# Kernel tuning notes

Measured on AMD Instinct MI355X. Metric: run time of the kernel, lower is better.

The kernel has to match this reference:

```python
import jax, jax.numpy as jnp
import numpy as np

STEPS, BATCH = 2048, 512
INPUT_DIM = 16          # climate features after stripping flow channel
STORE_DIM = 8           # number of conceptual stores S
HIDDEN = 128
SLOW = 2                # SLOW_STORE index
RAIN_IDX = 0            # rain column within sliced climate inputs
OUT_DIM = STORE_DIM * (STORE_DIM + 2)   # flow_between_stores=True -> 80
IN_DIM_FLOWNET = INPUT_DIM + STORE_DIM  # 24


def setup_inputs() -> dict:
    key = jax.random.key(0)
    ks = jax.random.split(key, 10)
    hyd_input = jax.random.uniform(ks[0], (STEPS, BATCH, 1 + INPUT_DIM), dtype=jnp.float32)
    s = 0.05
    W0 = jax.random.normal(ks[1], (HIDDEN, IN_DIM_FLOWNET), dtype=jnp.float32) * s
    b0 = jax.random.normal(ks[2], (HIDDEN,), dtype=jnp.float32) * s
    W1 = jax.random.normal(ks[3], (HIDDEN, HIDDEN), dtype=jnp.float32) * s
    b1 = jax.random.normal(ks[4], (HIDDEN,), dtype=jnp.float32) * s
    W_in = jax.random.normal(ks[5], (STORE_DIM + 1, HIDDEN), dtype=jnp.float32) * s
    b_in = jax.random.normal(ks[6], (STORE_DIM + 1,), dtype=jnp.float32) * s
    W_out = jax.random.normal(ks[7], (OUT_DIM, HIDDEN), dtype=jnp.float32) * s
    b_out = jax.random.normal(ks[8], (OUT_DIM,), dtype=jnp.float32) * s - 3.0  # bias.data -= 3
    return {"hyd_input": hyd_input, "W0": W0, "b0": b0, "W1": W1, "b1": b1,
            "W_in": W_in, "b_in": b_in, "W_out": W_out, "b_out": b_out}


def reference(hyd_input, W0, b0, W1, b1, W_in, b_in, W_out, b_out):
    S = STORE_DIM
    flow = hyd_input[:, :, 0]          # [T, B] observed flow
    x = hyd_input[:, :, 1:]            # [T, B, F] climate forcings
    rain = x[:, :, RAIN_IDX]           # [T, B]
    # correct_init_baseflow: 25th percentile of observed flow over time, per batch elem
    baseflow = jnp.percentile(flow, 25.0, axis=0)  # [B]

    B = x.shape[1]
    stores0 = jnp.zeros((B, S), dtype=hyd_input.dtype).at[:, 1].set(1.0)  # init_stores

    def step(stores, inp):
        x_t, rain_t, is_first = inp
        # flownet: (num_layers=2) Linear -> ReLU (dropout is eval-mode identity)
        h = jnp.concatenate([x_t, 0.01 * stores], axis=1)      # [B, F+S]
        h = jax.nn.relu(h @ W0.T + b0)
        h = jax.nn.relu(h @ W1.T + b1)
        # inflow gating (softmax over S+1): distribute rain into stores
        a = jax.nn.softmax(h @ W_in.T + b_in, axis=-1)          # [B, S+1]
        stores = stores + a[:, 1:] * rain_t[:, None]
        # outflow fluxes (sigmoid), S*(S+2) = inter-store | escape | flow
        b = jax.nn.sigmoid(h @ W_out.T + b_out)                 # [B, S*(S+2)]
        # sequential inter-store transfers (order matters; S is small/fixed)
        for d in range(S):
            fb = b[:, d * S:(d + 1) * S] * stores               # [B, S]
            stores = (stores - fb).at[:, d].add(fb.sum(axis=1))
        escape = b[:, -2 * S:-S] * stores
        stores = stores - escape
        b_flow = b[:, -S:]
        flow_distn = b_flow * stores
        stores = stores - flow_distn
        # at i==0: overwrite slow store from baseflow / outflow coeff
        corrected = stores.at[:, SLOW].set(baseflow / jnp.maximum(b_flow[:, SLOW], 1e-5))
        stores = jnp.where(is_first, corrected, stores)
        return stores, flow_distn.sum(axis=1)

    is_first = jnp.arange(x.shape[0]) == 0
    _, flows = jax.lax.scan(step, stores0, (x, rain, is_first))
    return flows  # [T, B]
```

## Files before the change

kernel.cpp:

```cpp
#include <hip/hip_runtime.h>
#include <hip/hip_bf16.h>
#include <math.h>

#define STEPS 2048
#define BATCH 512

typedef __attribute__((ext_vector_type(8))) short short8;
typedef __attribute__((ext_vector_type(4))) short short4v;
typedef __attribute__((ext_vector_type(2))) short short2v;
typedef __attribute__((ext_vector_type(4))) float f32x4;

__device__ __forceinline__ short f2bf(float f) {
    union { float f; unsigned u; } v; v.f = f;
    unsigned u = v.u;
    return (short)((u + 0x7FFFu + ((u >> 16) & 1u)) >> 16);
}
__device__ __forceinline__ short2v pk2(float a, float b) {
    __hip_bfloat162 h = __float22bfloat162_rn(make_float2(a, b));
    union { __hip_bfloat162 h; short2v s; } u; u.h = h; return u.s;
}

__global__ __launch_bounds__(256) void baseflow_kernel(
    const float* __restrict__ hyd, float* __restrict__ bf)
{
    __shared__ float arr[STEPS];
    const int b = blockIdx.x;
    const int tid = threadIdx.x;
    for (int t = tid; t < STEPS; t += 256)
        arr[t] = hyd[(size_t)(t * BATCH + b) * 17];
    __syncthreads();
    for (int k = 2; k <= STEPS; k <<= 1) {
        for (int j = k >> 1; j > 0; j >>= 1) {
            for (int i = tid; i < STEPS; i += 256) {
                int ixj = i ^ j;
                if (ixj > i) {
                    float a = arr[i], c = arr[ixj];
                    bool up = ((i & k) == 0);
                    if (up ? (a > c) : (a < c)) { arr[i] = c; arr[ixj] = a; }
                }
            }
            __syncthreads();
        }
    }
    if (tid == 0) bf[b] = arr[511] + 0.75f * (arr[512] - arr[511]);
}

__global__ __launch_bounds__(256, 1) void hyd_step_kernel(
    const float* __restrict__ hyd,
    const float* __restrict__ W0,  const float* __restrict__ b0,
    const float* __restrict__ W1,  const float* __restrict__ b1,
    const float* __restrict__ Win, const float* __restrict__ bin,
    const float* __restrict__ Wout,const float* __restrict__ bout,
    const float* __restrict__ baseflow,
    float* __restrict__ out)
{
    __shared__ __align__(16) short h1F[256 * 8];
    __shared__ __align__(16) short h2F[256 * 8];
    __shared__ __align__(16) short ringX[16 * 4 * 8];
    __shared__ float ringR[16][2];
    __shared__ __align__(16) float hb[2][96];

    const int tid  = threadIdx.x;
    const int blk  = blockIdx.x;
    const int lane = tid & 63;
    const int wv   = tid >> 6;
    const int cn   = lane & 15;
    const int cg   = lane >> 4;
    const int col  = lane & 1;

    for (int i = tid; i < 256 * 8; i += 256) { h1F[i] = 0; h2F[i] = 0; }

    short8 a0[2]; f32x4 c0[2];
    short8 a1[2][4]; f32x4 c1[2];
    short8 ah[2][4]; f32x4 ch[2];
    #pragma unroll
    for (int i = 0; i < 2; ++i) {
        const int mt = 2 * wv + i;
        const int row = mt * 16 + cn;
        #pragma unroll
        for (int j = 0; j < 8; ++j) {
            int k = cg * 8 + j;
            a0[i][j] = (k < 24) ? f2bf(W0[row * 24 + k]) : (short)0;
        }
        #pragma unroll
        for (int kt = 0; kt < 4; ++kt)
            #pragma unroll
            for (int j = 0; j < 8; ++j)
                a1[i][kt][j] = f2bf(W1[row * 128 + kt * 32 + cg * 8 + j]);
        #pragma unroll
        for (int r = 0; r < 4; ++r) {
            int m = mt * 16 + cg * 4 + r;
            c0[i][r] = b0[m];
            c1[i][r] = b1[m];
        }
    }
    const int nht = (wv < 2) ? 2 : 1;
    int htile[2];
    htile[0] = (wv < 2) ? 2 * wv : 4 + (wv - 2);
    htile[1] = (wv < 2) ? 2 * wv + 1 : htile[0];
    #pragma unroll
    for (int i = 0; i < 2; ++i) {
        const int ht = htile[i];
        const int row = ht * 16 + cn;
        #pragma unroll
        for (int kt = 0; kt < 4; ++kt)
            #pragma unroll
            for (int j = 0; j < 8; ++j) {
                int k = kt * 32 + cg * 8 + j;
                float w = 0.f;
                if (row < 9)       w = Win[row * 128 + k];
                else if (row < 89) w = Wout[(row - 9) * 128 + k];
                ah[i][kt][j] = f2bf(w);
            }
        #pragma unroll
        for (int r = 0; r < 4; ++r) {
            int m = ht * 16 + cg * 4 + r;
            float bb = 0.f;
            if (m < 9)       bb = bin[m];
            else if (m < 89) bb = bout[m - 9];
            ch[i][r] = bb;
        }
    }

    float sreg[8];
    #pragma unroll
    for (int j = 0; j < 8; ++j) sreg[j] = (j == 1) ? 1.f : 0.f;
    const float bfv = baseflow[blk * 2 + col];
    short8 spack;
    #pragma unroll
    for (int jj = 0; jj < 4; ++jj) {
        short2v p = pk2(0.01f * sreg[2 * jj], 0.01f * sreg[2 * jj + 1]);
        spack[2 * jj] = p[0]; spack[2 * jj + 1] = p[1];
    }

    for (int tb = 0; tb < STEPS; tb += 16) {
        if (tid < 64) {
            const int tp = tid >> 2, c = (tid >> 1) & 1, g2 = tid & 1;
            const float* p = hyd + ((size_t)(tb + tp) * BATCH + blk * 2 + c) * 17 + 1 + g2 * 8;
            float v0 = p[0], v1 = p[1], v2 = p[2], v3 = p[3];
            float v4 = p[4], v5 = p[5], v6 = p[6], v7 = p[7];
            short8 w;
            short2v q0 = pk2(v0, v1), q1 = pk2(v2, v3), q2 = pk2(v4, v5), q3 = pk2(v6, v7);
            w[0] = q0[0]; w[1] = q0[1]; w[2] = q1[0]; w[3] = q1[1];
            w[4] = q2[0]; w[5] = q2[1]; w[6] = q3[0]; w[7] = q3[1];
            *(short8*)&ringX[(tp * 4 + g2 * 2 + c) * 8] = w;
        } else if (tid < 96) {
            const int l = tid - 64, tp = l >> 1, c = l & 1;
            ringR[tp][c] = hyd[((size_t)(tb + tp) * BATCH + blk * 2 + c) * 17 + 1];
        }
        __syncthreads();

        for (int tt = 0; tt < 16; ++tt) {
            const int t = tb + tt;

            const float rain = ringR[tt][col];

            short8 bfrag = 0;
            if (cn < 2) {
                if (cg < 2)        bfrag = *(const short8*)&ringX[(tt * 4 + cg * 2 + cn) * 8];
                else if (cg == 2)  bfrag = spack;
            }
            #pragma unroll
            for (int i = 0; i < 2; ++i) {
                f32x4 acc = __builtin_amdgcn_mfma_f32_16x16x32_bf16(a0[i], bfrag, c0[i], 0, 0, 0);
                if (cn < 2) {
                    int m0 = (2 * wv + i) * 16 + cg * 4;
                    short4v p;
                    short2v pa = pk2(fmaxf(acc[0], 0.f), fmaxf(acc[1], 0.f));
                    short2v pb = pk2(fmaxf(acc[2], 0.f), fmaxf(acc[3], 0.f));
                    p[0] = pa[0]; p[1] = pa[1]; p[2] = pb[0]; p[3] = pb[1];
                    *(short4v*)&h1F[((m0 >> 3) * 16 + cn) * 8 + (m0 & 7)] = p;
                }
            }
            __syncthreads();

            short8 bf1[4];
            #pragma unroll
            for (int kt = 0; kt < 4; ++kt)
                bf1[kt] = *(const short8*)&h1F[(kt * 64 + lane) * 8];
            #pragma unroll
            for (int i = 0; i < 2; ++i) {
                f32x4 acc = c1[i];
                #pragma unroll
                for (int kt = 0; kt < 4; ++kt)
                    acc = __builtin_amdgcn_mfma_f32_16x16x32_bf16(a1[i][kt], bf1[kt], acc, 0, 0, 0);
                if (cn < 2) {
                    int m0 = (2 * wv + i) * 16 + cg * 4;
                    short4v p;
                    short2v pa = pk2(fmaxf(acc[0], 0.f), fmaxf(acc[1], 0.f));
                    short2v pb = pk2(fmaxf(acc[2], 0.f), fmaxf(acc[3], 0.f));
                    p[0] = pa[0]; p[1] = pa[1]; p[2] = pb[0]; p[3] = pb[1];
                    *(short4v*)&h2F[((m0 >> 3) * 16 + cn) * 8 + (m0 & 7)] = p;
                }
            }
            __syncthreads();

            short8 bf2[4];
            #pragma unroll
            for (int kt = 0; kt < 4; ++kt)
                bf2[kt] = *(const short8*)&h2F[(kt * 64 + lane) * 8];
            #pragma unroll
            for (int i = 0; i < 2; ++i) {
                if (i < nht) {
                    f32x4 acc = ch[i];
                    #pragma unroll
                    for (int kt = 0; kt < 4; ++kt)
                        acc = __builtin_amdgcn_mfma_f32_16x16x32_bf16(ah[i][kt], bf2[kt], acc, 0, 0, 0);
                    if (cn < 2) {
                        const int ht = htile[i];
                        float4 o;
                        #pragma unroll
                        for (int r = 0; r < 4; ++r) {
                            int m = ht * 16 + cg * 4 + r;
                            float v = acc[r];
                            bool isl = (m < 9);
                            float em = __expf(isl ? v : -v);
                            float res = isl ? em : __builtin_amdgcn_rcpf(1.f + em);
                            ((float*)&o)[r] = res;
                        }
                        *(float4*)&hb[cn][ht * 16 + cg * 4] = o;
                    }
                }
            }
            __syncthreads();

            {
                float gv[92];
                const float4* hp = (const float4*)&hb[col][0];
                #pragma unroll
                for (int c2 = 0; c2 < 23; ++c2)
                    ((float4*)gv)[c2] = hp[c2];

                float den = ((gv[0] + gv[1]) + (gv[2] + gv[3])) +
                            ((gv[4] + gv[5]) + (gv[6] + gv[7])) + gv[8];
                float rr = rain * __builtin_amdgcn_rcpf(den);
                #pragma unroll
                for (int j = 0; j < 8; ++j) sreg[j] += gv[1 + j] * rr;

                #pragma unroll
                for (int d = 0; d < 8; ++d) {
                    float fb[8];
                    #pragma unroll
                    for (int j = 0; j < 8; ++j) fb[j] = gv[9 + d * 8 + j] * sreg[j];
                    float fs = ((fb[0] + fb[1]) + (fb[2] + fb[3])) +
                               ((fb[4] + fb[5]) + (fb[6] + fb[7]));
                    #pragma unroll
                    for (int j = 0; j < 8; ++j) sreg[j] -= fb[j];
                    sreg[d] += fs;
                }
                #pragma unroll
                for (int j = 0; j < 8; ++j) sreg[j] -= gv[73 + j] * sreg[j];
                float fd[8];
                #pragma unroll
                for (int j = 0; j < 8; ++j) fd[j] = gv[81 + j] * sreg[j];
                float fsum = ((fd[0] + fd[1]) + (fd[2] + fd[3])) +
                             ((fd[4] + fd[5]) + (fd[6] + fd[7]));
                #pragma unroll
                for (int j = 0; j < 8; ++j) sreg[j] -= fd[j];
                if (t == 0) sreg[2] = bfv / fmaxf(gv[83], 1e-5f);

                #pragma unroll
                for (int jj = 0; jj < 4; ++jj) {
                    short2v p = pk2(0.01f * sreg[2 * jj], 0.01f * sreg[2 * jj + 1]);
                    spack[2 * jj] = p[0]; spack[2 * jj + 1] = p[1];
                }
                if (tid < 2) out[(size_t)t * BATCH + blk * 2 + tid] = fsum;
            }
        }
    }
}

extern "C" void kernel_launch(void* const* d_in, const int* in_sizes, int n_in,
                              void* d_out, int out_size, void* d_ws, size_t ws_size,
                              hipStream_t stream)
{
    const float* hyd  = (const float*)d_in[0];
    const float* W0   = (const float*)d_in[1];
    const float* b0   = (const float*)d_in[2];
    const float* W1   = (const float*)d_in[3];
    const float* b1   = (const float*)d_in[4];
    const float* Win  = (const float*)d_in[5];
    const float* bin  = (const float*)d_in[6];
    const float* Wout = (const float*)d_in[7];
    const float* bout = (const float*)d_in[8];
    float* out = (float*)d_out;
    float* bf  = (float*)d_ws;

    baseflow_kernel<<<BATCH, 256, 0, stream>>>(hyd, bf);
    hyd_step_kernel<<<BATCH / 2, 256, 0, stream>>>(
        hyd, W0, b0, W1, b1, Win, bin, Wout, bout, bf, out);
}
```

Baseline: 3.395 ms.

## Prefetch per-step inputs into registers and precompute input-layer MFMA off critical path

Drops the shared-memory ring buffer of 16 timesteps and its extra barrier. Each lane now prefetches the next step's climate inputs and rain straight into registers. The x-part of the first-layer MFMA for step t+1 is issued during step t's scalar store update, so only the store-dependent MFMA stays on the serial recurrence. The head weights are shifted by one row so the gate outputs line up for 2-wide float vector arithmetic (packed FMA) in the sequential store update. The cost is per-step global loads with latency that must be hidden, and more live registers.

```diff
diff --git a/kernel.cpp b/kernel.cpp
--- a/kernel.cpp
+++ b/kernel.cpp
@@ -9,6 +9,7 @@
 typedef __attribute__((ext_vector_type(4))) short short4v;
 typedef __attribute__((ext_vector_type(2))) short short2v;
 typedef __attribute__((ext_vector_type(4))) float f32x4;
+typedef __attribute__((ext_vector_type(2))) float f32x2;
 
 __device__ __forceinline__ short f2bf(float f) {
     union { float f; unsigned u; } v; v.f = f;
@@ -56,9 +57,7 @@
 {
     __shared__ __align__(16) short h1F[256 * 8];
     __shared__ __align__(16) short h2F[256 * 8];
-    __shared__ __align__(16) short ringX[16 * 4 * 8];
-    __shared__ float ringR[16][2];
-    __shared__ __align__(16) float hb[2][96];
+    __shared__ __align__(16) float hb[2][100];
 
     const int tid  = threadIdx.x;
     const int blk  = blockIdx.x;
@@ -108,164 +107,208 @@
             for (int j = 0; j < 8; ++j) {
                 int k = kt * 32 + cg * 8 + j;
                 float w = 0.f;
-                if (row < 9)       w = Win[row * 128 + k];
-                else if (row < 89) w = Wout[(row - 9) * 128 + k];
+                if (row != 1) {
+                    int q = (row == 0) ? 0 : (row - 1);
+                    if (q < 9)       w = Win[q * 128 + k];
+                    else if (q < 89) w = Wout[(q - 9) * 128 + k];
+                }
                 ah[i][kt][j] = f2bf(w);
             }
         #pragma unroll
         for (int r = 0; r < 4; ++r) {
             int m = ht * 16 + cg * 4 + r;
             float bb = 0.f;
-            if (m < 9)       bb = bin[m];
-            else if (m < 89) bb = bout[m - 9];
+            if (m != 1) {
+                int q = (m == 0) ? 0 : (m - 1);
+                if (q < 9)       bb = bin[q];
+                else if (q < 89) bb = bout[q - 9];
+            }
             ch[i][r] = bb;
         }
     }
 
-    float sreg[8];
-    #pragma unroll
-    for (int j = 0; j < 8; ++j) sreg[j] = (j == 1) ? 1.f : 0.f;
+    f32x2 s01 = {0.f, 1.f}, s23 = {0.f, 0.f}, s45 = {0.f, 0.f}, s67 = {0.f, 0.f};
     const float bfv = baseflow[blk * 2 + col];
     short8 spack;
-    #pragma unroll
-    for (int jj = 0; jj < 4; ++jj) {
-        short2v p = pk2(0.01f * sreg[2 * jj], 0.01f * sreg[2 * jj + 1]);
-        spack[2 * jj] = p[0]; spack[2 * jj + 1] = p[1];
-    }
-
-    for (int tb = 0; tb < STEPS; tb += 16) {
-        if (tid < 64) {
-            const int tp = tid >> 2, c = (tid >> 1) & 1, g2 = tid & 1;
-            const float* p = hyd + ((size_t)(tb + tp) * BATCH + blk * 2 + c) * 17 + 1 + g2 * 8;
-            float v0 = p[0], v1 = p[1], v2 = p[2], v3 = p[3];
-            float v4 = p[4], v5 = p[5], v6 = p[6], v7 = p[7];
-            short8 w;
-            short2v q0 = pk2(v0, v1), q1 = pk2(v2, v3), q2 = pk2(v4, v5), q3 = pk2(v6, v7);
-            w[0] = q0[0]; w[1] = q0[1]; w[2] = q1[0]; w[3] = q1[1];
-            w[4] = q2[0]; w[5] = q2[1]; w[6] = q3[0]; w[7] = q3[1];
-            *(short8*)&ringX[(tp * 4 + g2 * 2 + c) * 8] = w;
-        } else if (tid < 96) {
-            const int l = tid - 64, tp = l >> 1, c = l & 1;
-            ringR[tp][c] = hyd[((size_t)(tb + tp) * BATCH + blk * 2 + c) * 17 + 1];
+    {
+        short2v p0 = pk2(0.01f * s01.x, 0.01f * s01.y);
+        short2v p1 = pk2(0.01f * s23.x, 0.01f * s23.y);
+        short2v p2 = pk2(0.01f * s45.x, 0.01f * s45.y);
+        short2v p3 = pk2(0.01f * s67.x, 0.01f * s67.y);
+        spack[0] = p0[0]; spack[1] = p0[1]; spack[2] = p1[0]; spack[3] = p1[1];
+        spack[4] = p2[0]; spack[5] = p2[1]; spack[6] = p3[0]; spack[7] = p3[1];
+    }
+
+    const bool xlane = (cn < 2) && (cg < 2);
+    const int xoff = (blk * 2 + cn) * 17 + 1 + cg * 8;
+    const int roff = (blk * 2 + col) * 17 + 1;
+    float xv[8];
+    float rain_next;
+    if (xlane) {
+        const float* p = hyd + xoff;
+        #pragma unroll
+        for (int j = 0; j < 8; ++j) xv[j] = p[j];
+    }
+    rain_next = hyd[roff];
+
+    f32x4 accx0, accx1;
+    {
+        short8 xfrag = 0;
+        if (xlane) {
+            short2v q0 = pk2(xv[0], xv[1]), q1 = pk2(xv[2], xv[3]),
+                    q2 = pk2(xv[4], xv[5]), q3 = pk2(xv[6], xv[7]);
+            xfrag[0] = q0[0]; xfrag[1] = q0[1]; xfrag[2] = q1[0]; xfrag[3] = q1[1];
+            xfrag[4] = q2[0]; xfrag[5] = q2[1]; xfrag[6] = q3[0]; xfrag[7] = q3[1];
+        }
+        accx0 = __builtin_amdgcn_mfma_f32_16x16x32_bf16(a0[0], xfrag, c0[0], 0, 0, 0);
+        accx1 = __builtin_amdgcn_mfma_f32_16x16x32_bf16(a0[1], xfrag, c0[1], 0, 0, 0);
+    }
+
+    __syncthreads();
+
+    for (int t = 0; t < STEPS; ++t) {
+        const float rain = rain_next;
+        const int tn = (t + 1 < STEPS) ? (t + 1) : t;
+        const float* px = hyd + (size_t)tn * (BATCH * 17);
+        if (xlane) {
+            const float* p = px + xoff;
+            #pragma unroll
+            for (int j = 0; j < 8; ++j) xv[j] = p[j];
+        }
+        rain_next = px[roff];
+
+        short8 sfrag = 0;
+        if (cn < 2 && cg == 2) sfrag = spack;
+        #pragma unroll
+        for (int i = 0; i < 2; ++i) {
+            f32x4 acc = __builtin_amdgcn_mfma_f32_16x16x32_bf16(
+                a0[i], sfrag, (i ? accx1 : accx0), 0, 0, 0);
+            if (cn < 2) {
+                int m0 = (2 * wv + i) * 16 + cg * 4;
+                short4v p;
+                short2v pa = pk2(fmaxf(acc[0], 0.f), fmaxf(acc[1], 0.f));
+                short2v pb = pk2(fmaxf(acc[2], 0.f), fmaxf(acc[3], 0.f));
+                p[0] = pa[0]; p[1] = pa[1]; p[2] = pb[0]; p[3] = pb[1];
+                *(short4v*)&h1F[((m0 >> 3) * 16 + cn) * 8 + (m0 & 7)] = p;
+            }
         }
         __syncthreads();
 
-        for (int tt = 0; tt < 16; ++tt) {
-            const int t = tb + tt;
-
-            const float rain = ringR[tt][col];
-
-            short8 bfrag = 0;
+        short8 bf1[4];
+        #pragma unroll
+        for (int kt = 0; kt < 4; ++kt)
+            bf1[kt] = *(const short8*)&h1F[(kt * 64 + lane) * 8];
+        #pragma unroll
+        for (int i = 0; i < 2; ++i) {
+            f32x4 acc = c1[i];
+            #pragma unroll
+            for (int kt = 0; kt < 4; ++kt)
+                acc = __builtin_amdgcn_mfma_f32_16x16x32_bf16(a1[i][kt], bf1[kt], acc, 0, 0, 0);
             if (cn < 2) {
-                if (cg < 2)        bfrag = *(const short8*)&ringX[(tt * 4 + cg * 2 + cn) * 8];
-                else if (cg == 2)  bfrag = spack;
-            }
-            #pragma unroll
-            for (int i = 0; i < 2; ++i) {
-                f32x4 acc = __builtin_amdgcn_mfma_f32_16x16x32_bf16(a0[i], bfrag, c0[i], 0, 0, 0);
-                if (cn < 2) {
-                    int m0 = (2 * wv + i) * 16 + cg * 4;
-                    short4v p;
-                    short2v pa = pk2(fmaxf(acc[0], 0.f), fmaxf(acc[1], 0.f));
-                    short2v pb = pk2(fmaxf(acc[2], 0.f), fmaxf(acc[3], 0.f));
-                    p[0] = pa[0]; p[1] = pa[1]; p[2] = pb[0]; p[3] = pb[1];
-                    *(short4v*)&h1F[((m0 >> 3) * 16 + cn) * 8 + (m0 & 7)] = p;
-                }
-            }
-            __syncthreads();
-
-            short8 bf1[4];
-            #pragma unroll
-            for (int kt = 0; kt < 4; ++kt)
-                bf1[kt] = *(const short8*)&h1F[(kt * 64 + lane) * 8];
-            #pragma unroll
-            for (int i = 0; i < 2; ++i) {
-                f32x4 acc = c1[i];
+                int m0 = (2 * wv + i) * 16 + cg * 4;
+                short4v p;
+                short2v pa = pk2(fmaxf(acc[0], 0.f), fmaxf(acc[1], 0.f));
+                short2v pb = pk2(fmaxf(acc[2], 0.f), fmaxf(acc[3], 0.f));
+                p[0] = pa[0]; p[1] = pa[1]; p[2] = pb[0]; p[3] = pb[1];
+                *(short4v*)&h2F[((m0 >> 3) * 16 + cn) * 8 + (m0 & 7)] = p;
+            }
+        }
+        __syncthreads();
+
+        short8 bf2[4];
+        #pragma unroll
+        for (int kt = 0; kt < 4; ++kt)
+            bf2[kt] = *(const short8*)&h2F[(kt * 64 + lane) * 8];
+        #pragma unroll
+        for (int i = 0; i < 2; ++i) {
+            if (i < nht) {
+                f32x4 acc = ch[i];
                 #pragma unroll
                 for (int kt = 0; kt < 4; ++kt)
-                    acc = __builtin_amdgcn_mfma_f32_16x16x32_bf16(a1[i][kt], bf1[kt], acc, 0, 0, 0);
+                    acc = __builtin_amdgcn_mfma_f32_16x16x32_bf16(ah[i][kt], bf2[kt], acc, 0, 0, 0);
                 if (cn < 2) {
-                    int m0 = (2 * wv + i) * 16 + cg * 4;
-                    short4v p;
-                    short2v pa = pk2(fmaxf(acc[0], 0.f), fmaxf(acc[1], 0.f));
-                    short2v pb = pk2(fmaxf(acc[2], 0.f), fmaxf(acc[3], 0.f));
-                    p[0] = pa[0]; p[1] = pa[1]; p[2] = pb[0]; p[3] = pb[1];
-                    *(short4v*)&h2F[((m0 >> 3) * 16 + cn) * 8 + (m0 & 7)] = p;
+                    const int ht = htile[i];
+                    float4 o;
+                    #pragma unroll
+                    for (int r = 0; r < 4; ++r) {
+                        int m = ht * 16 + cg * 4 + r;
+                        float v = acc[r];
+                        bool isl = (m < 10);
+                        float em = __expf(isl ? v : -v);
+                        float res = isl ? em : __builtin_amdgcn_rcpf(1.f + em);
+                        ((float*)&o)[r] = res;
+                    }
+                    *(float4*)&hb[cn][ht * 16 + cg * 4] = o;
                 }
             }
-            __syncthreads();
-
-            short8 bf2[4];
-            #pragma unroll
-            for (int kt = 0; kt < 4; ++kt)
-                bf2[kt] = *(const short8*)&h2F[(kt * 64 + lane) * 8];
-            #pragma unroll
-            for (int i = 0; i < 2; ++i) {
-                if (i < nht) {
-                    f32x4 acc = ch[i];
-                    #pragma unroll
-                    for (int kt = 0; kt < 4; ++kt)
-                        acc = __builtin_amdgcn_mfma_f32_16x16x32_bf16(ah[i][kt], bf2[kt], acc, 0, 0, 0);
-                    if (cn < 2) {
-                        const int ht = htile[i];
-                        float4 o;
-                        #pragma unroll
-                        for (int r = 0; r < 4; ++r) {
-                            int m = ht * 16 + cg * 4 + r;
-                            float v = acc[r];
-                            bool isl = (m < 9);
-                            float em = __expf(isl ? v : -v);
-                            float res = isl ? em : __builtin_amdgcn_rcpf(1.f + em);
-                            ((float*)&o)[r] = res;
-                        }
-                        *(float4*)&hb[cn][ht * 16 + cg * 4] = o;
-                    }
-                }
-            }
-            __syncthreads();
+        }
+        __syncthreads();
+
+        float4 gq[23];
+        {
+            const float4* hp = (const float4*)&hb[col][0];
+            #pragma unroll
+            for (int c2 = 0; c2 < 23; ++c2) gq[c2] = hp[c2];
+        }
+
+        {
+            short8 xfrag = 0;
+            if (xlane) {
+                short2v q0 = pk2(xv[0], xv[1]), q1 = pk2(xv[2], xv[3]),
+                        q2 = pk2(xv[4], xv[5]), q3 = pk2(xv[6], xv[7]);
+                xfrag[0] = q0[0]; xfrag[1] = q0[1]; xfrag[2] = q1[0]; xfrag[3] = q1[1];
+                xfrag[4] = q2[0]; xfrag[5] = q2[1]; xfrag[6] = q3[0]; xfrag[7] = q3[1];
+            }
+            accx0 = __builtin_amdgcn_mfma_f32_16x16x32_bf16(a0[0], xfrag, c0[0], 0, 0, 0);
+            accx1 = __builtin_amdgcn_mfma_f32_16x16x32_bf16(a0[1], xfrag, c0[1], 0, 0, 0);
+        }
+
+        {
+            const f32x2* g2 = (const f32x2*)gq;
+            const float* gv = (const float*)gq;
+
+            f32x2 dt = (g2[1] + g2[2]) + (g2[3] + g2[4]);
+            float den = gv[0] + dt.x + dt.y;
+            float rr = rain * __builtin_amdgcn_rcpf(den);
+            f32x2 rr2 = {rr, rr};
+            s01 += g2[1] * rr2; s23 += g2[2] * rr2;
+            s45 += g2[3] * rr2; s67 += g2[4] * rr2;
+
+            #pragma unroll
+            for (int d = 0; d < 8; ++d) {
+                const int gb = 5 + 4 * d;
+                f32x2 fb0 = g2[gb + 0] * s01, fb1 = g2[gb + 1] * s23;
+                f32x2 fb2 = g2[gb + 2] * s45, fb3 = g2[gb + 3] * s67;
+                f32x2 tt = (fb0 + fb1) + (fb2 + fb3);
+                float fs = tt.x + tt.y;
+                s01 -= fb0; s23 -= fb1; s45 -= fb2; s67 -= fb3;
+                if      (d == 0) s01.x += fs;
+                else if (d == 1) s01.y += fs;
+                else if (d == 2) s23.x += fs;
+                else if (d == 3) s23.y += fs;
+                else if (d == 4) s45.x += fs;
+                else if (d == 5) s45.y += fs;
+                else if (d == 6) s67.x += fs;
+                else             s67.y += fs;
+            }
+            s01 -= g2[37] * s01; s23 -= g2[38] * s23;
+            s45 -= g2[39] * s45; s67 -= g2[40] * s67;
+            f32x2 f0 = g2[41] * s01, f1 = g2[42] * s23;
+            f32x2 f2 = g2[43] * s45, f3 = g2[44] * s67;
+            f32x2 ft = (f0 + f1) + (f2 + f3);
+            float fsum = ft.x + ft.y;
+            s01 -= f0; s23 -= f1; s45 -= f2; s67 -= f3;
+            if (t == 0) s23.x = bfv / fmaxf(gv[84], 1e-5f);
 
             {
-                float gv[92];
-                const float4* hp = (const float4*)&hb[col][0];
-                #pragma unroll
-                for (int c2 = 0; c2 < 23; ++c2)
-                    ((float4*)gv)[c2] = hp[c2];
-
-                float den = ((gv[0] + gv[1]) + (gv[2] + gv[3])) +
-                            ((gv[4] + gv[5]) + (gv[6] + gv[7])) + gv[8];
-                float rr = rain * __builtin_amdgcn_rcpf(den);
-                #pragma unroll
-                for (int j = 0; j < 8; ++j) sreg[j] += gv[1 + j] * rr;
-
-                #pragma unroll
-                for (int d = 0; d < 8; ++d) {
-                    float fb[8];
-                    #pragma unroll
-                    for (int j = 0; j < 8; ++j) fb[j] = gv[9 + d * 8 + j] * sreg[j];
-                    float fs = ((fb[0] + fb[1]) + (fb[2] + fb[3])) +
-                               ((fb[4] + fb[5]) + (fb[6] + fb[7]));
-                    #pragma unroll
-                    for (int j = 0; j < 8; ++j) sreg[j] -= fb[j];
-                    sreg[d] += fs;
-                }
-                #pragma unroll
-                for (int j = 0; j < 8; ++j) sreg[j] -= gv[73 + j] * sreg[j];
-                float fd[8];
-                #pragma unroll
-                for (int j = 0; j < 8; ++j) fd[j] = gv[81 + j] * sreg[j];
-                float fsum = ((fd[0] + fd[1]) + (fd[2] + fd[3])) +
-                             ((fd[4] + fd[5]) + (fd[6] + fd[7]));
-                #pragma unroll
-                for (int j = 0; j < 8; ++j) sreg[j] -= fd[j];
-                if (t == 0) sreg[2] = bfv / fmaxf(gv[83], 1e-5f);
-
-                #pragma unroll
-                for (int jj = 0; jj < 4; ++jj) {
-                    short2v p = pk2(0.01f * sreg[2 * jj], 0.01f * sreg[2 * jj + 1]);
-                    spack[2 * jj] = p[0]; spack[2 * jj + 1] = p[1];
-                }
-                if (tid < 2) out[(size_t)t * BATCH + blk * 2 + tid] = fsum;
-            }
+                short2v p0 = pk2(0.01f * s01.x, 0.01f * s01.y);
+                short2v p1 = pk2(0.01f * s23.x, 0.01f * s23.y);
+                short2v p2 = pk2(0.01f * s45.x, 0.01f * s45.y);
+                short2v p3 = pk2(0.01f * s67.x, 0.01f * s67.y);
+                spack[0] = p0[0]; spack[1] = p0[1]; spack[2] = p1[0]; spack[3] = p1[1];
+                spack[4] = p2[0]; spack[5] = p2[1]; spack[6] = p3[0]; spack[7] = p3[1];
+            }
+            if (tid < 2) out[(size_t)t * BATCH + blk * 2 + tid] = fsum;
         }
     }
 }
```

Result: faster. 3.072 ms (-9.5%).
